# Optimization experiments

Measured on AMD Instinct MI355X. Metric: run time of the kernel, lower is better.

## Reference

```python
import jax, jax.numpy as jnp
import numpy as np

N_NODES = 50000
N_EDGES = 1_600_000
N_GRAPHS = 64
EMB = 1280
GCN_DIMS = [128, 256, 256]
FC_DIMS = [1024, 128]
EPS = 1e-5  # BatchNorm eps (torch default)


def setup_inputs() -> dict:
    key = jax.random.key(0)
    ks = jax.random.split(key, 16)
    inp = {}
    inp["x"] = jax.random.normal(ks[0], (N_NODES, EMB), jnp.float32)
    inp["edge_index"] = jax.random.randint(ks[1], (2, N_EDGES), 0, N_NODES)
    inp["batch"] = jnp.sort(jax.random.randint(ks[2], (N_NODES,), 0, N_GRAPHS))
    dims = [EMB] + GCN_DIMS
    for i in range(3):
        inp[f"Wg{i}"] = jax.random.normal(ks[3 + i], (dims[i], dims[i + 1]), jnp.float32) * (1.0 / np.sqrt(dims[i]))
        inp[f"bg{i}"] = jnp.zeros((dims[i + 1],), jnp.float32)
        inp[f"gamma{i}"] = jnp.ones((dims[i + 1],), jnp.float32)
        inp[f"beta{i}"] = jnp.zeros((dims[i + 1],), jnp.float32)
    fdims = [GCN_DIMS[-1]] + FC_DIMS
    for i in range(2):
        inp[f"Wf{i}"] = jax.random.normal(ks[10 + i], (fdims[i], fdims[i + 1]), jnp.float32) * (1.0 / np.sqrt(fdims[i]))
        inp[f"bf{i}"] = jnp.zeros((fdims[i + 1],), jnp.float32)
    return inp


def _batchnorm(h, gamma, beta):
    # training-mode BN over node dim, biased variance (torch normalization)
    m = h.mean(axis=0)
    v = h.var(axis=0)
    return gamma * (h - m) * jax.lax.rsqrt(v + EPS) + beta


def reference(x, edge_index, batch,
              Wg0, bg0, gamma0, beta0,
              Wg1, bg1, gamma1, beta1,
              Wg2, bg2, gamma2, beta2,
              Wf0, bf0, Wf1, bf1):
    # --- GCN symmetric normalization with self-loops (PyG GCNConv default) ---
    loop = jnp.arange(N_NODES)
    src = jnp.concatenate([edge_index[0], loop])  # message sources
    dst = jnp.concatenate([edge_index[1], loop])  # aggregation targets
    deg = jax.ops.segment_sum(jnp.ones(src.shape[0], jnp.float32), dst, num_segments=N_NODES)
    dinv = jnp.where(deg > 0, jax.lax.rsqrt(jnp.maximum(deg, 1.0)), 0.0)
    norm = dinv[src] * dinv[dst]  # [E + N]

    def gcn_conv(h, W, b):
        h = h @ W                               # [N, d_out] transform first (PyG order)
        msg = h[src] * norm[:, None]            # gather + scale
        return jax.ops.segment_sum(msg, dst, num_segments=N_NODES) + b

    h = x
    for W, b, g, bt in ((Wg0, bg0, gamma0, beta0),
                        (Wg1, bg1, gamma1, beta1),
                        (Wg2, bg2, gamma2, beta2)):
        h = gcn_conv(h, W, b)
        h = _batchnorm(h, g, bt)
        h = jax.nn.relu(h)
        # dropout is identity in eval mode

    # --- global mean pool over graphs ---
    counts = jax.ops.segment_sum(jnp.ones(N_NODES, jnp.float32), batch, num_segments=N_GRAPHS)
    sums = jax.ops.segment_sum(h, batch, num_segments=N_GRAPHS)
    g = sums / jnp.maximum(counts, 1.0)[:, None]  # [B, 256]

    # --- FC head ---
    g = jax.nn.relu(g @ Wf0 + bf0)
    out = g @ Wf1 + bf1                           # [B, 128]
    return out
```

## Files before the change

### kernel.cpp

```cpp
#include <hip/hip_runtime.h>
#include <hip/hip_bf16.h>

#define N_NODES 50000
#define N_EDGES 1600000
#define N_GRAPHS 64
#define MT_TILES 1563

typedef _Float16 f16;
typedef _Float16 f16x8 __attribute__((ext_vector_type(8)));
typedef _Float16 f16x4 __attribute__((ext_vector_type(4)));
typedef _Float16 f16x2 __attribute__((ext_vector_type(2)));
typedef float f32x4 __attribute__((ext_vector_type(4)));

template <int V> struct VecT;
template <> struct VecT<2> { using type = f16x2; };
template <> struct VecT<4> { using type = f16x4; };

__global__ void init_deg(int* deg) {
    int i = blockIdx.x * blockDim.x + threadIdx.x;
    if (i < N_NODES) deg[i] = 1;
}

__global__ void deg_count(const int* __restrict__ dst, int* __restrict__ deg) {
    int e = blockIdx.x * blockDim.x + threadIdx.x;
    if (e < N_EDGES) atomicAdd(&deg[dst[e]], 1);
}

__global__ void make_dinv(const int* __restrict__ deg, float* __restrict__ dinv) {
    int i = blockIdx.x * blockDim.x + threadIdx.x;
    if (i < N_NODES) dinv[i] = rsqrtf((float)deg[i]);
}

__global__ void scan_deg(const int* __restrict__ deg, int* __restrict__ rowstart,
                         int* __restrict__ pos) {
    __shared__ int wsum[16];
    __shared__ int carry_s;
    const int t = threadIdx.x;
    const int lane = t & 63;
    const int w = t >> 6;
    if (t == 0) carry_s = 0;
    __syncthreads();
    for (int base = 0; base < N_NODES; base += 1024) {
        int i = base + t;
        int v = (i < N_NODES) ? (deg[i] - 1) : 0;
        int s = v;
#pragma unroll
        for (int off = 1; off < 64; off <<= 1) {
            int n = __shfl_up(s, off, 64);
            if (lane >= off) s += n;
        }
        if (lane == 63) wsum[w] = s;
        __syncthreads();
        if (w == 0) {
            int ws = (lane < 16) ? wsum[lane] : 0;
#pragma unroll
            for (int off = 1; off < 16; off <<= 1) {
                int n = __shfl_up(ws, off, 64);
                if (lane >= off) ws += n;
            }
            if (lane < 16) wsum[lane] = ws;
        }
        __syncthreads();
        int waveoff = (w == 0) ? 0 : wsum[w - 1];
        int carry = carry_s;
        int excl = carry + waveoff + s - v;
        if (i < N_NODES) {
            rowstart[i] = excl;
            pos[i] = excl;
        }
        __syncthreads();
        if (t == 0) carry_s = carry + wsum[15];
        __syncthreads();
    }
    if (t == 0) rowstart[N_NODES] = carry_s;
}

__global__ void csr_fill(const int* __restrict__ src, const int* __restrict__ dst,
                         const float* __restrict__ dinv, int* __restrict__ pos,
                         int2* __restrict__ csr) {
    int e = blockIdx.x * blockDim.x + threadIdx.x;
    if (e >= N_EDGES) return;
    int s = src[e], d = dst[e];
    int slot = atomicAdd(&pos[d], 1);
    csr[slot] = make_int2(s, __float_as_int(dinv[s] * dinv[d]));
}

__global__ void cast_w(const float* __restrict__ W, f16* __restrict__ Wt, int K, int N) {
    int i = blockIdx.x * blockDim.x + threadIdx.x;
    if (i >= K * N) return;
    int k = i % K, n = i / K;
    Wt[i] = (f16)W[(size_t)k * N + n];
}

__launch_bounds__(256)
__global__ void cast_x_blocked(const float* __restrict__ x, f16* __restrict__ xb) {
    const int mt = blockIdx.x;
    const int t = threadIdx.x;
    const size_t base = (size_t)mt * 32 * 1280;
    const size_t tbase = (size_t)mt * 40 * 1024;
#pragma unroll 4
    for (int i = 0; i < 40; ++i) {
        int f = i * 1024 + t * 4;
        int r = f / 1280;
        int k = f - r * 1280;
        float4 v = make_float4(0.f, 0.f, 0.f, 0.f);
        if (mt * 32 + r < N_NODES) v = *(const float4*)(x + base + f);
        int kt = k >> 5, kk = k & 31;
        f16x4 o = {(f16)v.x, (f16)v.y, (f16)v.z, (f16)v.w};
        *(f16x4*)(xb + tbase + (size_t)kt * 1024 + r * 32 + kk) = o;
    }
}

__launch_bounds__(256)
__global__ void gemm_xb_f16_sk(const f16* __restrict__ xb, const f16* __restrict__ Bt,
                               float* __restrict__ C0, float* __restrict__ C1, int M) {
    const int K = 1280;
    const int gw = (int)((blockIdx.x * blockDim.x + threadIdx.x) >> 6);
    const int lane = threadIdx.x & 63;
    const int mt = gw >> 1, s = gw & 1;
    const int m0 = mt * 32;
    if (m0 >= M) return;
    float* __restrict__ C = s ? C1 : C0;
    const int r = lane & 15, q = lane >> 4;
    const f16* at = xb + (size_t)mt * 40 * 1024 + (size_t)s * 20 * 1024 + r * 32 + q * 8;
    const f16* bp = Bt + (size_t)r * K + s * 640 + q * 8;

    f32x4 acc[2][8];
#pragma unroll
    for (int i = 0; i < 2; ++i)
#pragma unroll
        for (int j = 0; j < 8; ++j) acc[i][j] = (f32x4){0.f, 0.f, 0.f, 0.f};

#pragma unroll 2
    for (int kt = 0; kt < 20; ++kt) {
        f16x8 a0 = *(const f16x8*)(at + kt * 1024);
        f16x8 a1 = *(const f16x8*)(at + kt * 1024 + 512);
#pragma unroll
        for (int ni = 0; ni < 8; ++ni) {
            f16x8 bf = *(const f16x8*)(bp + (size_t)ni * 16 * K + kt * 32);
            acc[0][ni] = __builtin_amdgcn_mfma_f32_16x16x32_f16(a0, bf, acc[0][ni], 0, 0, 0);
            acc[1][ni] = __builtin_amdgcn_mfma_f32_16x16x32_f16(a1, bf, acc[1][ni], 0, 0, 0);
        }
    }
#pragma unroll
    for (int mi = 0; mi < 2; ++mi)
#pragma unroll
        for (int j = 0; j < 4; ++j) {
            int row = m0 + mi * 16 + q * 4 + j;
            if (row < M) {
                float* cp = C + (size_t)row * 128 + r;
#pragma unroll
                for (int ni = 0; ni < 8; ++ni) cp[ni * 16] = acc[mi][ni][j];
            }
        }
}

__global__ void reduce_cast(const float* __restrict__ c0, const float* __restrict__ c1,
                            f16* __restrict__ o, int n4) {
    int i = blockIdx.x * blockDim.x + threadIdx.x;
    if (i >= n4) return;
    float4 a = ((const float4*)c0)[i];
    float4 b = ((const float4*)c1)[i];
    f16x4 r = {(f16)(a.x + b.x), (f16)(a.y + b.y), (f16)(a.z + b.z), (f16)(a.w + b.w)};
    ((f16x4*)o)[i] = r;
}

template <int K>
__launch_bounds__(256)
__global__ void gemm_h_f16(const f16* __restrict__ A16, const f16* __restrict__ Bt,
                           f16* __restrict__ C16, int M, int N) {
    const int wave = (int)((blockIdx.x * blockDim.x + threadIdx.x) >> 6);
    const int lane = threadIdx.x & 63;
    const int m0 = wave * 32;
    if (m0 >= M) return;
    const int col0 = blockIdx.y * 128;
    const int r = lane & 15, q = lane >> 4;
    int row0 = m0 + r;       int row0c = row0 < M ? row0 : M - 1;
    int row1 = m0 + 16 + r;  int row1c = row1 < M ? row1 : M - 1;
    const f16* a0 = A16 + (size_t)row0c * K + q * 8;
    const f16* a1 = A16 + (size_t)row1c * K + q * 8;
    const f16* bp = Bt + (size_t)(col0 + r) * K + q * 8;

    f32x4 acc[2][8];
#pragma unroll
    for (int i = 0; i < 2; ++i)
#pragma unroll
        for (int j = 0; j < 8; ++j) acc[i][j] = (f32x4){0.f, 0.f, 0.f, 0.f};

#pragma unroll
    for (int k0 = 0; k0 < K; k0 += 32) {
        f16x8 af0 = *(const f16x8*)(a0 + k0);
        f16x8 af1 = *(const f16x8*)(a1 + k0);
#pragma unroll
        for (int ni = 0; ni < 8; ++ni) {
            f16x8 bf = *(const f16x8*)(bp + (size_t)ni * 16 * K + k0);
            acc[0][ni] = __builtin_amdgcn_mfma_f32_16x16x32_f16(af0, bf, acc[0][ni], 0, 0, 0);
            acc[1][ni] = __builtin_amdgcn_mfma_f32_16x16x32_f16(af1, bf, acc[1][ni], 0, 0, 0);
        }
    }
#pragma unroll
    for (int mi = 0; mi < 2; ++mi)
#pragma unroll
        for (int j = 0; j < 4; ++j) {
            int row = m0 + mi * 16 + q * 4 + j;
            if (row < M) {
                f16* cp = C16 + (size_t)row * N + col0 + r;
#pragma unroll
                for (int ni = 0; ni < 8; ++ni) cp[ni * 16] = (f16)acc[mi][ni][j];
            }
        }
}

template <int D>
__launch_bounds__(256)
__global__ void aggregate(const f16* __restrict__ h, const int* __restrict__ rowstart,
                          const int2* __restrict__ csr, const float* __restrict__ dinv,
                          const float* __restrict__ bias, f16* __restrict__ out) {
    constexpr int V = D / 64;
    using vec = typename VecT<V>::type;
    int w = (int)((blockIdx.x * blockDim.x + threadIdx.x) >> 6);
    int lane = threadIdx.x & 63;
    if (w >= N_NODES) return;
    float acc[V];
    float di = dinv[w];
    vec self = *(const vec*)(h + (size_t)w * D + lane * V);
#pragma unroll
    for (int v = 0; v < V; ++v) acc[v] = (float)self[v] * (di * di);
    int e0 = rowstart[w], e1 = rowstart[w + 1];
    int j = e0;
    for (; j + 8 <= e1; j += 8) {
        int2 c[8];
        vec rr[8];
#pragma unroll
        for (int u = 0; u < 8; ++u) c[u] = csr[j + u];
#pragma unroll
        for (int u = 0; u < 8; ++u)
            rr[u] = *(const vec*)(h + (size_t)c[u].x * D + lane * V);
#pragma unroll
        for (int u = 0; u < 8; ++u) {
            float nm = __int_as_float(c[u].y);
#pragma unroll
            for (int v = 0; v < V; ++v) acc[v] += (float)rr[u][v] * nm;
        }
    }
    if (j + 4 <= e1) {
        int2 c0 = csr[j], c1 = csr[j + 1], c2 = csr[j + 2], c3 = csr[j + 3];
        vec r0 = *(const vec*)(h + (size_t)c0.x * D + lane * V);
        vec r1 = *(const vec*)(h + (size_t)c1.x * D + lane * V);
        vec r2 = *(const vec*)(h + (size_t)c2.x * D + lane * V);
        vec r3 = *(const vec*)(h + (size_t)c3.x * D + lane * V);
        float n0 = __int_as_float(c0.y), n1 = __int_as_float(c1.y);
        float n2 = __int_as_float(c2.y), n3 = __int_as_float(c3.y);
#pragma unroll
        for (int v = 0; v < V; ++v)
            acc[v] += (float)r0[v] * n0 + (float)r1[v] * n1 +
                      (float)r2[v] * n2 + (float)r3[v] * n3;
        j += 4;
    }
    for (; j < e1; ++j) {
        int2 c = csr[j];
        vec r = *(const vec*)(h + (size_t)c.x * D + lane * V);
        float nm = __int_as_float(c.y);
#pragma unroll
        for (int v = 0; v < V; ++v) acc[v] += (float)r[v] * nm;
    }
    vec o;
#pragma unroll
    for (int v = 0; v < V; ++v) o[v] = (f16)(acc[v] + bias[lane * V + v]);
    *(vec*)(out + (size_t)w * D + lane * V) = o;
}

template <int D>
__global__ void bn_stats(const f16* __restrict__ h, float* __restrict__ stat) {
    int f = threadIdx.x;
    int r0 = blockIdx.x * 128;
    int r1 = min(r0 + 128, N_NODES);
    float s = 0.f, s2 = 0.f;
    for (int r = r0; r < r1; ++r) {
        float v = (float)h[(size_t)r * D + f];
        s += v;
        s2 += v * v;
    }
    atomicAdd(&stat[f], s);
    atomicAdd(&stat[D + f], s2);
}

template <int D>
__global__ void bn_finalize(const float* __restrict__ stat, const float* __restrict__ gamma,
                            const float* __restrict__ beta, float* __restrict__ ss) {
    int f = threadIdx.x;
    float m = stat[f] * (1.0f / N_NODES);
    float var = stat[D + f] * (1.0f / N_NODES) - m * m;
    float sc = gamma[f] * rsqrtf(var + 1e-5f);
    ss[f] = sc;
    ss[D + f] = beta[f] - m * sc;
}

template <int D>
__global__ void bn_apply_relu(const f16* __restrict__ hin, const float* __restrict__ ss,
                              f16* __restrict__ hout) {
    int i = blockIdx.x * blockDim.x + threadIdx.x;
    if (i >= N_NODES * D / 8) return;
    int f0 = (i * 8) & (D - 1);
    f16x8 v = ((const f16x8*)hin)[i];
    f16x8 r;
#pragma unroll
    for (int j = 0; j < 8; ++j) {
        float val = (float)v[j] * ss[f0 + j] + ss[D + f0 + j];
        r[j] = (f16)(val > 0.f ? val : 0.f);
    }
    ((f16x8*)hout)[i] = r;
}

__global__ void count_batch_bs(const int* __restrict__ batch, int* __restrict__ cnt) {
    int g = threadIdx.x;
    if (g >= N_GRAPHS) return;
    int lo = 0, hi = N_NODES;
    while (lo < hi) { int mid = (lo + hi) >> 1; if (batch[mid] < g) lo = mid + 1; else hi = mid; }
    int b0 = lo;
    lo = 0; hi = N_NODES;
    while (lo < hi) { int mid = (lo + hi) >> 1; if (batch[mid] < g + 1) lo = mid + 1; else hi = mid; }
    cnt[g] = lo - b0;
}

__global__ void pool_seg(const f16* __restrict__ h, const int* __restrict__ batch,
                         float* __restrict__ psum) {
    int f = threadIdx.x;
    int r0 = blockIdx.x * 64;
    int r1 = min(r0 + 64, N_NODES);
    float acc = 0.f;
    int cur = batch[r0];
    for (int r = r0; r < r1; ++r) {
        int b = batch[r];
        if (b != cur) {
            atomicAdd(&psum[cur * 256 + f], acc);
            acc = 0.f;
            cur = b;
        }
        acc += (float)h[(size_t)r * 256 + f];
    }
    atomicAdd(&psum[cur * 256 + f], acc);
}

__global__ void pool_div(const float* __restrict__ psum, const int* __restrict__ cnt,
                         float* __restrict__ g) {
    int i = blockIdx.x * 256 + threadIdx.x;
    int b = i >> 8;
    float c = (float)max(cnt[b], 1);
    g[i] = psum[i] / c;
}

__global__ void fc_init(const float* __restrict__ b, float* __restrict__ Y, int rows, int N) {
    int i = blockIdx.x * blockDim.x + threadIdx.x;
    if (i < rows * N) Y[i] = b[i % N];
}

__global__ void fc_splitk(const float* __restrict__ X, const float* __restrict__ W,
                          float* __restrict__ Y, int K, int N, int KC) {
    int col = blockIdx.x * blockDim.x + threadIdx.x;
    int row = blockIdx.y;
    int k0 = blockIdx.z * KC;
    float acc = 0.f;
    const float* x = X + (size_t)row * K + k0;
    const float* w = W + (size_t)k0 * N + col;
#pragma unroll 8
    for (int k = 0; k < KC; ++k) acc += x[k] * w[(size_t)k * N];
    atomicAdd(&Y[(size_t)row * N + col], acc);
}

__global__ void relu_inplace(float* __restrict__ Y, int n) {
    int i = blockIdx.x * blockDim.x + threadIdx.x;
    if (i < n) Y[i] = Y[i] > 0.f ? Y[i] : 0.f;
}

extern "C" void kernel_launch(void* const* d_in, const int* in_sizes, int n_in,
                              void* d_out, int out_size, void* d_ws, size_t ws_size,
                              hipStream_t stream) {
    const float* x     = (const float*)d_in[0];
    const int*   ei    = (const int*)d_in[1];
    const int*   batch = (const int*)d_in[2];
    const float* Wg0 = (const float*)d_in[3],  *bg0 = (const float*)d_in[4];
    const float* gamma0 = (const float*)d_in[5], *beta0 = (const float*)d_in[6];
    const float* Wg1 = (const float*)d_in[7],  *bg1 = (const float*)d_in[8];
    const float* gamma1 = (const float*)d_in[9], *beta1 = (const float*)d_in[10];
    const float* Wg2 = (const float*)d_in[11], *bg2 = (const float*)d_in[12];
    const float* gamma2 = (const float*)d_in[13], *beta2 = (const float*)d_in[14];
    const float* Wf0 = (const float*)d_in[15], *bf0 = (const float*)d_in[16];
    const float* Wf1 = (const float*)d_in[17], *bf1 = (const float*)d_in[18];
    float* out = (float*)d_out;

    size_t off = 0;
    auto alloc = [&](size_t bytes) {
        void* p = (char*)d_ws + off;
        off += (bytes + 255) & ~(size_t)255;
        return p;
    };
    f16*   hA16     = (f16*)alloc((size_t)N_NODES * 256 * 2);
    float* cp32     = (float*)alloc((size_t)2 * N_NODES * 128 * 4);
    f16*   hBn16    = (f16*)cp32;
    f16*   h16      = (f16*)(cp32 + (size_t)N_NODES * 128);
    float* cp0      = cp32;
    float* cp1      = cp32 + (size_t)N_NODES * 128;
    f16*   xb       = (f16*)alloc((size_t)MT_TILES * 40 * 1024 * 2);
    int2*  csr      = (int2*)alloc((size_t)N_EDGES * 8);
    int*   deg      = (int*)alloc((size_t)N_NODES * 4);
    float* dinv     = (float*)alloc((size_t)N_NODES * 4);
    int*   rowstart = (int*)alloc((size_t)(N_NODES + 1) * 4);
    int*   pos      = (int*)alloc((size_t)N_NODES * 4);
    float* bnstat   = (float*)alloc(2 * 256 * 4);
    float* bnss     = (float*)alloc(2 * 256 * 4);
    float* psum     = (float*)alloc(64 * 256 * 4);
    int*   pcount   = (int*)alloc(64 * 4);
    float* gpool    = (float*)alloc(64 * 256 * 4);
    float* g1       = (float*)alloc(64 * 1024 * 4);
    f16*   W0t      = (f16*)alloc((size_t)1280 * 128 * 2);
    f16*   W1t      = (f16*)alloc((size_t)128 * 256 * 2);
    f16*   W2t      = (f16*)alloc((size_t)256 * 256 * 2);
    (void)ws_size;

    const int TPB = 256;
    const int nb_nodes = (N_NODES + TPB - 1) / TPB;
    const int nb_edges = (N_EDGES + TPB - 1) / TPB;

    cast_x_blocked<<<MT_TILES, TPB, 0, stream>>>(x, xb);
    init_deg<<<nb_nodes, TPB, 0, stream>>>(deg);
    deg_count<<<nb_edges, TPB, 0, stream>>>(ei + N_EDGES, deg);
    make_dinv<<<nb_nodes, TPB, 0, stream>>>(deg, dinv);
    scan_deg<<<1, 1024, 0, stream>>>(deg, rowstart, pos);
    csr_fill<<<nb_edges, TPB, 0, stream>>>(ei, ei + N_EDGES, dinv, pos, csr);
    cast_w<<<(1280 * 128 + 255) / 256, 256, 0, stream>>>(Wg0, W0t, 1280, 128);
    cast_w<<<(128 * 256 + 255) / 256, 256, 0, stream>>>(Wg1, W1t, 128, 256);
    cast_w<<<(256 * 256 + 255) / 256, 256, 0, stream>>>(Wg2, W2t, 256, 256);

    const int gemm_blocks = ((N_NODES + 31) / 32 * 64 + TPB - 1) / TPB;
    const int gemm_sk_blocks = (MT_TILES * 2 * 64 + TPB - 1) / TPB;
    const int agg_blocks = (N_NODES * 64 + TPB - 1) / TPB;

    gemm_xb_f16_sk<<<gemm_sk_blocks, TPB, 0, stream>>>(xb, W0t, cp0, cp1, N_NODES);
    reduce_cast<<<(N_NODES * 128 / 4 + 255) / 256, 256, 0, stream>>>(cp0, cp1, hA16, N_NODES * 128 / 4);
    aggregate<128><<<agg_blocks, TPB, 0, stream>>>(hA16, rowstart, csr, dinv, bg0, hBn16);
    hipMemsetAsync(bnstat, 0, 2 * 128 * 4, stream);
    bn_stats<128><<<(N_NODES + 127) / 128, 128, 0, stream>>>(hBn16, bnstat);
    bn_finalize<128><<<1, 128, 0, stream>>>(bnstat, gamma0, beta0, bnss);
    bn_apply_relu<128><<<(N_NODES * 128 / 8 + 255) / 256, 256, 0, stream>>>(hBn16, bnss, h16);

    gemm_h_f16<128><<<dim3(gemm_blocks, 2), TPB, 0, stream>>>(h16, W1t, hA16, N_NODES, 256);
    aggregate<256><<<agg_blocks, TPB, 0, stream>>>(hA16, rowstart, csr, dinv, bg1, hBn16);
    hipMemsetAsync(bnstat, 0, 2 * 256 * 4, stream);
    bn_stats<256><<<(N_NODES + 127) / 128, 256, 0, stream>>>(hBn16, bnstat);
    bn_finalize<256><<<1, 256, 0, stream>>>(bnstat, gamma1, beta1, bnss);
    bn_apply_relu<256><<<(N_NODES * 256 / 8 + 255) / 256, 256, 0, stream>>>(hBn16, bnss, h16);

    gemm_h_f16<256><<<dim3(gemm_blocks, 2), TPB, 0, stream>>>(h16, W2t, hA16, N_NODES, 256);
    aggregate<256><<<agg_blocks, TPB, 0, stream>>>(hA16, rowstart, csr, dinv, bg2, hBn16);
    hipMemsetAsync(bnstat, 0, 2 * 256 * 4, stream);
    bn_stats<256><<<(N_NODES + 127) / 128, 256, 0, stream>>>(hBn16, bnstat);
    bn_finalize<256><<<1, 256, 0, stream>>>(bnstat, gamma2, beta2, bnss);
    bn_apply_relu<256><<<(N_NODES * 256 / 8 + 255) / 256, 256, 0, stream>>>(hBn16, bnss, h16);

    hipMemsetAsync(psum, 0, 64 * 256 * 4, stream);
    count_batch_bs<<<1, 64, 0, stream>>>(batch, pcount);
    pool_seg<<<(N_NODES + 63) / 64, 256, 0, stream>>>(h16, batch, psum);
    pool_div<<<64, 256, 0, stream>>>(psum, pcount, gpool);

    fc_init<<<(64 * 1024 + 255) / 256, 256, 0, stream>>>(bf0, g1, 64, 1024);
    fc_splitk<<<dim3(4, 64, 4), 256, 0, stream>>>(gpool, Wf0, g1, 256, 1024, 64);
    relu_inplace<<<(64 * 1024 + 255) / 256, 256, 0, stream>>>(g1, 64 * 1024);
    fc_init<<<(64 * 128 + 255) / 256, 256, 0, stream>>>(bf1, out, 64, 128);
    fc_splitk<<<dim3(1, 64, 16), 128, 0, stream>>>(g1, Wf1, out, 1024, 128, 64);
}
```

Baseline: 947.8 us.

## Fuse BN-apply+ReLU into following GEMMs and pooling; shrink GEMM wave tiles to 16 rows

Removes the three standalone bn_apply_relu passes by applying the BatchNorm scale/shift and ReLU on the fly when loading A operands in the hidden-layer GEMMs and inside the pooling kernel. This avoids writing and re-reading a full normalized activation tensor per layer. The GEMM kernels also change to one 16-row M tile per wave instead of 32, which doubles the number of waves and halves B-operand reuse per wave. BN math is now repeated across the two column blocks of the hidden GEMMs.

Measured after the change: 1.003 ms. +5.8%, slower.

```diff
diff --git a/kernel.cpp b/kernel.cpp
--- a/kernel.cpp
+++ b/kernel.cpp
@@ -113,46 +113,38 @@
 
 __launch_bounds__(256)
 __global__ void gemm_xb_f16_sk(const f16* __restrict__ xb, const f16* __restrict__ Bt,
-                               float* __restrict__ C0, float* __restrict__ C1, int M) {
+                               float* __restrict__ C0, float* __restrict__ C1) {
     const int K = 1280;
     const int gw = (int)((blockIdx.x * blockDim.x + threadIdx.x) >> 6);
+    if (gw >= 6250) return;
     const int lane = threadIdx.x & 63;
-    const int mt = gw >> 1, s = gw & 1;
-    const int m0 = mt * 32;
-    if (m0 >= M) return;
+    const int m16 = gw >> 1, s = gw & 1;
+    const int mt = m16 >> 1, half = m16 & 1;
     float* __restrict__ C = s ? C1 : C0;
     const int r = lane & 15, q = lane >> 4;
-    const f16* at = xb + (size_t)mt * 40 * 1024 + (size_t)s * 20 * 1024 + r * 32 + q * 8;
+    const f16* at = xb + (size_t)mt * 40960 + (size_t)s * 20480 + half * 512 + r * 32 + q * 8;
     const f16* bp = Bt + (size_t)r * K + s * 640 + q * 8;
 
-    f32x4 acc[2][8];
-#pragma unroll
-    for (int i = 0; i < 2; ++i)
-#pragma unroll
-        for (int j = 0; j < 8; ++j) acc[i][j] = (f32x4){0.f, 0.f, 0.f, 0.f};
-
-#pragma unroll 2
+    f32x4 acc[8];
+#pragma unroll
+    for (int j = 0; j < 8; ++j) acc[j] = (f32x4){0.f, 0.f, 0.f, 0.f};
+
+#pragma unroll 4
     for (int kt = 0; kt < 20; ++kt) {
-        f16x8 a0 = *(const f16x8*)(at + kt * 1024);
-        f16x8 a1 = *(const f16x8*)(at + kt * 1024 + 512);
+        f16x8 a = *(const f16x8*)(at + kt * 1024);
 #pragma unroll
         for (int ni = 0; ni < 8; ++ni) {
             f16x8 bf = *(const f16x8*)(bp + (size_t)ni * 16 * K + kt * 32);
-            acc[0][ni] = __builtin_amdgcn_mfma_f32_16x16x32_f16(a0, bf, acc[0][ni], 0, 0, 0);
-            acc[1][ni] = __builtin_amdgcn_mfma_f32_16x16x32_f16(a1, bf, acc[1][ni], 0, 0, 0);
-        }
-    }
-#pragma unroll
-    for (int mi = 0; mi < 2; ++mi)
-#pragma unroll
-        for (int j = 0; j < 4; ++j) {
-            int row = m0 + mi * 16 + q * 4 + j;
-            if (row < M) {
-                float* cp = C + (size_t)row * 128 + r;
-#pragma unroll
-                for (int ni = 0; ni < 8; ++ni) cp[ni * 16] = acc[mi][ni][j];
-            }
-        }
+            acc[ni] = __builtin_amdgcn_mfma_f32_16x16x32_f16(a, bf, acc[ni], 0, 0, 0);
+        }
+    }
+#pragma unroll
+    for (int j = 0; j < 4; ++j) {
+        int row = m16 * 16 + q * 4 + j;
+        float* cp = C + (size_t)row * 128 + r;
+#pragma unroll
+        for (int ni = 0; ni < 8; ++ni) cp[ni * 16] = acc[ni][j];
+    }
 }
 
 __global__ void reduce_cast(const float* __restrict__ c0, const float* __restrict__ c1,
@@ -167,48 +159,44 @@
 
 template <int K>
 __launch_bounds__(256)
-__global__ void gemm_h_f16(const f16* __restrict__ A16, const f16* __restrict__ Bt,
-                           f16* __restrict__ C16, int M, int N) {
-    const int wave = (int)((blockIdx.x * blockDim.x + threadIdx.x) >> 6);
+__global__ void gemm_h_bn_f16(const f16* __restrict__ A16, const float* __restrict__ ss,
+                              const f16* __restrict__ Bt, f16* __restrict__ C16, int N) {
+    const int gw = (int)((blockIdx.x * blockDim.x + threadIdx.x) >> 6);
+    if (gw >= N_NODES / 16) return;
     const int lane = threadIdx.x & 63;
-    const int m0 = wave * 32;
-    if (m0 >= M) return;
+    const int m0 = gw * 16;
     const int col0 = blockIdx.y * 128;
     const int r = lane & 15, q = lane >> 4;
-    int row0 = m0 + r;       int row0c = row0 < M ? row0 : M - 1;
-    int row1 = m0 + 16 + r;  int row1c = row1 < M ? row1 : M - 1;
-    const f16* a0 = A16 + (size_t)row0c * K + q * 8;
-    const f16* a1 = A16 + (size_t)row1c * K + q * 8;
+    const f16* a0 = A16 + (size_t)(m0 + r) * K + q * 8;
     const f16* bp = Bt + (size_t)(col0 + r) * K + q * 8;
 
-    f32x4 acc[2][8];
-#pragma unroll
-    for (int i = 0; i < 2; ++i)
-#pragma unroll
-        for (int j = 0; j < 8; ++j) acc[i][j] = (f32x4){0.f, 0.f, 0.f, 0.f};
+    f32x4 acc[8];
+#pragma unroll
+    for (int j = 0; j < 8; ++j) acc[j] = (f32x4){0.f, 0.f, 0.f, 0.f};
 
 #pragma unroll
     for (int k0 = 0; k0 < K; k0 += 32) {
-        f16x8 af0 = *(const f16x8*)(a0 + k0);
-        f16x8 af1 = *(const f16x8*)(a1 + k0);
+        f16x8 raw = *(const f16x8*)(a0 + k0);
+        const int kb = k0 + q * 8;
+        f16x8 af;
+#pragma unroll
+        for (int j = 0; j < 8; ++j) {
+            float v = (float)raw[j] * ss[kb + j] + ss[K + kb + j];
+            af[j] = (f16)(v > 0.f ? v : 0.f);
+        }
 #pragma unroll
         for (int ni = 0; ni < 8; ++ni) {
             f16x8 bf = *(const f16x8*)(bp + (size_t)ni * 16 * K + k0);
-            acc[0][ni] = __builtin_amdgcn_mfma_f32_16x16x32_f16(af0, bf, acc[0][ni], 0, 0, 0);
-            acc[1][ni] = __builtin_amdgcn_mfma_f32_16x16x32_f16(af1, bf, acc[1][ni], 0, 0, 0);
-        }
-    }
-#pragma unroll
-    for (int mi = 0; mi < 2; ++mi)
-#pragma unroll
-        for (int j = 0; j < 4; ++j) {
-            int row = m0 + mi * 16 + q * 4 + j;
-            if (row < M) {
-                f16* cp = C16 + (size_t)row * N + col0 + r;
-#pragma unroll
-                for (int ni = 0; ni < 8; ++ni) cp[ni * 16] = (f16)acc[mi][ni][j];
-            }
-        }
+            acc[ni] = __builtin_amdgcn_mfma_f32_16x16x32_f16(af, bf, acc[ni], 0, 0, 0);
+        }
+    }
+#pragma unroll
+    for (int j = 0; j < 4; ++j) {
+        int row = m0 + q * 4 + j;
+        f16* cp = C16 + (size_t)row * N + col0 + r;
+#pragma unroll
+        for (int ni = 0; ni < 8; ++ni) cp[ni * 16] = (f16)acc[ni][j];
+    }
 }
 
 template <int D>
@@ -296,22 +284,6 @@
     ss[D + f] = beta[f] - m * sc;
 }
 
-template <int D>
-__global__ void bn_apply_relu(const f16* __restrict__ hin, const float* __restrict__ ss,
-                              f16* __restrict__ hout) {
-    int i = blockIdx.x * blockDim.x + threadIdx.x;
-    if (i >= N_NODES * D / 8) return;
-    int f0 = (i * 8) & (D - 1);
-    f16x8 v = ((const f16x8*)hin)[i];
-    f16x8 r;
-#pragma unroll
-    for (int j = 0; j < 8; ++j) {
-        float val = (float)v[j] * ss[f0 + j] + ss[D + f0 + j];
-        r[j] = (f16)(val > 0.f ? val : 0.f);
-    }
-    ((f16x8*)hout)[i] = r;
-}
-
 __global__ void count_batch_bs(const int* __restrict__ batch, int* __restrict__ cnt) {
     int g = threadIdx.x;
     if (g >= N_GRAPHS) return;
@@ -323,9 +295,10 @@
     cnt[g] = lo - b0;
 }
 
-__global__ void pool_seg(const f16* __restrict__ h, const int* __restrict__ batch,
-                         float* __restrict__ psum) {
+__global__ void pool_seg_bn(const f16* __restrict__ h, const float* __restrict__ ss,
+                            const int* __restrict__ batch, float* __restrict__ psum) {
     int f = threadIdx.x;
+    float sc = ss[f], sh = ss[256 + f];
     int r0 = blockIdx.x * 64;
     int r1 = min(r0 + 64, N_NODES);
     float acc = 0.f;
@@ -337,7 +310,8 @@
             acc = 0.f;
             cur = b;
         }
-        acc += (float)h[(size_t)r * 256 + f];
+        float v = sc * (float)h[(size_t)r * 256 + f] + sh;
+        acc += v > 0.f ? v : 0.f;
     }
     atomicAdd(&psum[cur * 256 + f], acc);
 }
@@ -398,7 +372,6 @@
     f16*   hA16     = (f16*)alloc((size_t)N_NODES * 256 * 2);
     float* cp32     = (float*)alloc((size_t)2 * N_NODES * 128 * 4);
     f16*   hBn16    = (f16*)cp32;
-    f16*   h16      = (f16*)(cp32 + (size_t)N_NODES * 128);
     float* cp0      = cp32;
     float* cp1      = cp32 + (size_t)N_NODES * 128;
     f16*   xb       = (f16*)alloc((size_t)MT_TILES * 40 * 1024 * 2);
@@ -432,35 +405,32 @@
     cast_w<<<(128 * 256 + 255) / 256, 256, 0, stream>>>(Wg1, W1t, 128, 256);
     cast_w<<<(256 * 256 + 255) / 256, 256, 0, stream>>>(Wg2, W2t, 256, 256);
 
-    const int gemm_blocks = ((N_NODES + 31) / 32 * 64 + TPB - 1) / TPB;
-    const int gemm_sk_blocks = (MT_TILES * 2 * 64 + TPB - 1) / TPB;
+    const int gemm0_blocks = (6250 * 64 + TPB - 1) / TPB;
+    const int gemmh_blocks = (N_NODES / 16 * 64 + TPB - 1) / TPB;
     const int agg_blocks = (N_NODES * 64 + TPB - 1) / TPB;
 
-    gemm_xb_f16_sk<<<gemm_sk_blocks, TPB, 0, stream>>>(xb, W0t, cp0, cp1, N_NODES);
+    gemm_xb_f16_sk<<<gemm0_blocks, TPB, 0, stream>>>(xb, W0t, cp0, cp1);
     reduce_cast<<<(N_NODES * 128 / 4 + 255) / 256, 256, 0, stream>>>(cp0, cp1, hA16, N_NODES * 128 / 4);
     aggregate<128><<<agg_blocks, TPB, 0, stream>>>(hA16, rowstart, csr, dinv, bg0, hBn16);
     hipMemsetAsync(bnstat, 0, 2 * 128 * 4, stream);
     bn_stats<128><<<(N_NODES + 127) / 128, 128, 0, stream>>>(hBn16, bnstat);
     bn_finalize<128><<<1, 128, 0, stream>>>(bnstat, gamma0, beta0, bnss);
-    bn_apply_relu<128><<<(N_NODES * 128 / 8 + 255) / 256, 256, 0, stream>>>(hBn16, bnss, h16);
-
-    gemm_h_f16<128><<<dim3(gemm_blocks, 2), TPB, 0, stream>>>(h16, W1t, hA16, N_NODES, 256);
+
+    gemm_h_bn_f16<128><<<dim3(gemmh_blocks, 2), TPB, 0, stream>>>(hBn16, bnss, W1t, hA16, 256);
     aggregate<256><<<agg_blocks, TPB, 0, stream>>>(hA16, rowstart, csr, dinv, bg1, hBn16);
     hipMemsetAsync(bnstat, 0, 2 * 256 * 4, stream);
     bn_stats<256><<<(N_NODES + 127) / 128, 256, 0, stream>>>(hBn16, bnstat);
     bn_finalize<256><<<1, 256, 0, stream>>>(bnstat, gamma1, beta1, bnss);
-    bn_apply_relu<256><<<(N_NODES * 256 / 8 + 255) / 256, 256, 0, stream>>>(hBn16, bnss, h16);
-
-    gemm_h_f16<256><<<dim3(gemm_blocks, 2), TPB, 0, stream>>>(h16, W2t, hA16, N_NODES, 256);
+
+    gemm_h_bn_f16<256><<<dim3(gemmh_blocks, 2), TPB, 0, stream>>>(hBn16, bnss, W2t, hA16, 256);
     aggregate<256><<<agg_blocks, TPB, 0, stream>>>(hA16, rowstart, csr, dinv, bg2, hBn16);
     hipMemsetAsync(bnstat, 0, 2 * 256 * 4, stream);
     bn_stats<256><<<(N_NODES + 127) / 128, 256, 0, stream>>>(hBn16, bnstat);
     bn_finalize<256><<<1, 256, 0, stream>>>(bnstat, gamma2, beta2, bnss);
-    bn_apply_relu<256><<<(N_NODES * 256 / 8 + 255) / 256, 256, 0, stream>>>(hBn16, bnss, h16);
 
     hipMemsetAsync(psum, 0, 64 * 256 * 4, stream);
     count_batch_bs<<<1, 64, 0, stream>>>(batch, pcount);
-    pool_seg<<<(N_NODES + 63) / 64, 256, 0, stream>>>(h16, batch, psum);
+    pool_seg_bn<<<(N_NODES + 63) / 64, 256, 0, stream>>>(hBn16, bnss, batch, psum);
     pool_div<<<64, 256, 0, stream>>>(psum, pcount, gpool);
 
     fc_init<<<(64 * 1024 + 255) / 256, 256, 0, stream>>>(bf0, g1, 64, 1024);
```
